# Performance work log

Hardware: AMD Instinct MI355X
Metric: run time of the kernel (lower is better)

The kernel has to match this reference:

```python
import jax, jax.numpy as jnp
import numpy as np

EMBED_DIM = 1024
NUM_HEADS = 16
HEAD_DIM = EMBED_DIM // NUM_HEADS  # 64
KERNEL_SIZE = 64


def apply_rotary_emb(x, freqs_cos, freqs_sin):
    # x: [B, L, H, D]; freqs: [L, D//2]
    x_r = x[..., 0::2]
    x_i = x[..., 1::2]
    cos = freqs_cos[None, :, None, :]
    sin = freqs_sin[None, :, None, :]
    out_r = x_r * cos - x_i * sin
    out_i = x_r * sin + x_i * cos
    return jnp.stack([out_r, out_i], axis=-1).reshape(x.shape)


def setup_inputs() -> dict:
    key = jax.random.key(0)
    ks = jax.random.split(key, 8)
    B, L = 4, 4096
    x = jax.random.normal(ks[0], (B, L, EMBED_DIM), dtype=jnp.float32)
    freqs_cos = jax.random.normal(ks[1], (L, HEAD_DIM // 2), dtype=jnp.float32)
    freqs_sin = jax.random.normal(ks[2], (L, HEAD_DIM // 2), dtype=jnp.float32)
    attention_mask = jnp.ones((B, L), dtype=jnp.float32)
    scale = 1.0 / np.sqrt(EMBED_DIM)
    Wqkv = jax.random.normal(ks[3], (EMBED_DIM, 3 * EMBED_DIM), dtype=jnp.float32) * scale
    bqkv = jnp.zeros((3 * EMBED_DIM,), dtype=jnp.float32)
    proj = jax.random.normal(ks[4], (NUM_HEADS, HEAD_DIM, KERNEL_SIZE), dtype=jnp.float32) / np.sqrt(HEAD_DIM)
    Wout = jax.random.normal(ks[5], (EMBED_DIM, EMBED_DIM), dtype=jnp.float32) * scale
    bout = jnp.zeros((EMBED_DIM,), dtype=jnp.float32)
    return {"x": x, "freqs_cos": freqs_cos, "freqs_sin": freqs_sin,
            "attention_mask": attention_mask, "Wqkv": Wqkv, "bqkv": bqkv,
            "proj": proj, "Wout": Wout, "bout": bout}


def reference(x, freqs_cos, freqs_sin, attention_mask, Wqkv, bqkv, proj, Wout, bout):
    B, L, E = x.shape
    H, D = NUM_HEADS, HEAD_DIM
    qkv = x @ Wqkv + bqkv  # [B, L, 3E]
    q, k, v = jnp.split(qkv, 3, axis=-1)
    q = q.reshape(B, L, H, D)
    k = k.reshape(B, L, H, D)
    v = v.reshape(B, L, H, D)
    q = apply_rotary_emb(q, freqs_cos, freqs_sin)
    k = apply_rotary_emb(k, freqs_cos, freqs_sin)
    q = q.transpose(0, 2, 1, 3)  # [B, H, L, D]
    k = k.transpose(0, 2, 1, 3)
    v = v.transpose(0, 2, 1, 3)
    q_prime = jax.nn.relu(jnp.einsum('bhld,hdm->bhlm', q, proj))
    k_prime = jax.nn.relu(jnp.einsum('bhld,hdm->bhlm', k, proj))
    mask = attention_mask[:, None, :, None]  # [B, 1, L, 1]
    k_prime = k_prime * mask
    v = v * mask
    kv = jnp.einsum('bhlm,bhld->bhmd', k_prime, v)      # [B, H, M, D]
    context = jnp.einsum('bhlm,bhmd->bhld', q_prime, kv)  # [B, H, L, D]
    k_sum = k_prime.sum(axis=2)  # [B, H, M]
    norm = jnp.einsum('bhlm,bhm->bhl', q_prime, k_sum)
    output = context / (norm[..., None] + 0.0001)
    output = output.transpose(0, 2, 1, 3).reshape(B, L, E)
    return output @ Wout + bout
```

## Files before the change

kernel.cpp:

```cpp
#include <hip/hip_runtime.h>

#define LSEQ   4096
#define ROWS   16384
#define EMBED  1024
#define NHEADS 16
#define HDIM   64
#define QKV_N  3072

typedef __attribute__((ext_vector_type(8))) short bf16x8;
typedef __attribute__((ext_vector_type(8))) unsigned short u16x8;
typedef __attribute__((ext_vector_type(4))) float f32x4;
typedef __attribute__((ext_vector_type(16))) float f32x16;

__device__ inline unsigned short bf16_rne(float x) {
    unsigned int u = __float_as_uint(x);
    unsigned int r = (u + 0x7fffu + ((u >> 16) & 1u)) >> 16;
    return (unsigned short)r;
}
__device__ inline float bf16_to_f32(unsigned short h) {
    return __uint_as_float(((unsigned int)h) << 16);
}

__device__ __forceinline__ int swz64(int row, int s) {
    return row * 64 + ((((s >> 3) ^ (row & 7))) << 3) + (s & 7);
}

__global__ __launch_bounds__(256)
void convert_hilo(const float* __restrict__ in, unsigned short* __restrict__ hi,
                  unsigned short* __restrict__ lo, int n)
{
    int i = (blockIdx.x * 256 + threadIdx.x) << 2;
    if (i >= n) return;
    float4 v = *reinterpret_cast<const float4*>(&in[i]);
    float a[4] = {v.x, v.y, v.z, v.w};
    unsigned short hh[4], ll[4];
    #pragma unroll
    for (int j = 0; j < 4; ++j) {
        hh[j] = bf16_rne(a[j]);
        ll[j] = bf16_rne(a[j] - bf16_to_f32(hh[j]));
    }
    *reinterpret_cast<ushort4*>(&hi[i]) = make_ushort4(hh[0], hh[1], hh[2], hh[3]);
    *reinterpret_cast<ushort4*>(&lo[i]) = make_ushort4(ll[0], ll[1], ll[2], ll[3]);
}

__global__ __launch_bounds__(256)
void convert_T_hilo(const float* __restrict__ in, unsigned short* __restrict__ hi,
                    unsigned short* __restrict__ lo, int K, int N)
{
    __shared__ float tile[64][65];
    const int n0 = blockIdx.x * 64, k0 = blockIdx.y * 64;
    const int t = threadIdx.x;
    #pragma unroll
    for (int i = 0; i < 16; ++i) {
        int idx = t + i * 256;
        int r = idx >> 6, c = idx & 63;
        tile[r][c] = in[(size_t)(k0 + r) * N + n0 + c];
    }
    __syncthreads();
    #pragma unroll
    for (int i = 0; i < 16; ++i) {
        int idx = t + i * 256;
        int r = idx >> 6, c = idx & 63;
        float v = tile[c][r];
        unsigned short h = bf16_rne(v);
        unsigned short l = bf16_rne(v - bf16_to_f32(h));
        size_t o = (size_t)(n0 + r) * K + k0 + c;
        hi[o] = h;
        lo[o] = l;
    }
}

__global__ __launch_bounds__(256)
void gemm3_kernel(const unsigned short* __restrict__ Ah, const unsigned short* __restrict__ Al,
                  const unsigned short* __restrict__ Bh, const unsigned short* __restrict__ Bl,
                  const float* __restrict__ bias, float* __restrict__ C,
                  int K, int ldc)
{
    __shared__ __align__(16) unsigned short lds[2][16384];

    const int t = threadIdx.x;
    const int wave = t >> 6, lane = t & 63;
    const int wr = wave >> 1, wc = wave & 1;
    const int rowBase = blockIdx.y * 128;
    const int colBase = blockIdx.x * 128;
    const int l31 = lane & 31, kg = lane >> 5;

    const unsigned short* src = (wave == 0) ? Ah : (wave == 1) ? Al : (wave == 2) ? Bh : Bl;
    const int tileRow0 = (wave < 2) ? rowBase : colBase;
    const int ldsOff = wave * 4096;
    const int sRow = lane >> 2;
    const int sChunk = (((lane & 3) ^ ((lane >> 3) & 3)) << 3);

    f32x16 acc[2][2] = {};
    const int NT = K >> 5;

    #pragma unroll
    for (int i = 0; i < 8; ++i) {
        const unsigned short* g = src + (size_t)(tileRow0 + i * 16 + sRow) * K + sChunk;
        __builtin_amdgcn_global_load_lds(
            (const __attribute__((address_space(1))) void*)g,
            (__attribute__((address_space(3))) void*)&lds[0][ldsOff + i * 512], 16, 0, 0);
    }
    __syncthreads();

    for (int tI = 0; tI < NT; ++tI) {
        const int cur = tI & 1;

        if (tI + 1 < NT) {
            const int k0 = (tI + 1) << 5;
            #pragma unroll
            for (int i = 0; i < 8; ++i) {
                const unsigned short* g =
                    src + (size_t)(tileRow0 + i * 16 + sRow) * K + k0 + sChunk;
                __builtin_amdgcn_global_load_lds(
                    (const __attribute__((address_space(1))) void*)g,
                    (__attribute__((address_space(3))) void*)&lds[cur ^ 1][ldsOff + i * 512], 16, 0, 0);
            }
        }

        bf16x8 ah[2][2], al[2][2], bh[2][2], bl[2][2];
        #pragma unroll
        for (int ks = 0; ks < 2; ++ks) {
            #pragma unroll
            for (int m = 0; m < 2; ++m) {
                int r = wr * 64 + m * 32 + l31;
                int off = r * 32 + ((((ks << 1) | kg) ^ ((r >> 1) & 3)) << 3);
                ah[ks][m] = *reinterpret_cast<const bf16x8*>(&lds[cur][off]);
                al[ks][m] = *reinterpret_cast<const bf16x8*>(&lds[cur][4096 + off]);
            }
            #pragma unroll
            for (int n = 0; n < 2; ++n) {
                int rb = wc * 64 + n * 32 + l31;
                int off = rb * 32 + ((((ks << 1) | kg) ^ ((rb >> 1) & 3)) << 3);
                bh[ks][n] = *reinterpret_cast<const bf16x8*>(&lds[cur][8192 + off]);
                bl[ks][n] = *reinterpret_cast<const bf16x8*>(&lds[cur][12288 + off]);
            }
        }
        #pragma unroll
        for (int ks = 0; ks < 2; ++ks)
            #pragma unroll
            for (int m = 0; m < 2; ++m)
                #pragma unroll
                for (int n = 0; n < 2; ++n) {
                    acc[m][n] = __builtin_amdgcn_mfma_f32_32x32x16_bf16(ah[ks][m], bh[ks][n], acc[m][n], 0, 0, 0);
                    acc[m][n] = __builtin_amdgcn_mfma_f32_32x32x16_bf16(ah[ks][m], bl[ks][n], acc[m][n], 0, 0, 0);
                    acc[m][n] = __builtin_amdgcn_mfma_f32_32x32x16_bf16(al[ks][m], bh[ks][n], acc[m][n], 0, 0, 0);
                }

        __syncthreads();
    }

    #pragma unroll
    for (int n = 0; n < 2; ++n) {
        const int col = colBase + wc * 64 + n * 32 + l31;
        const float bv = bias[col];
        #pragma unroll
        for (int m = 0; m < 2; ++m) {
            #pragma unroll
            for (int reg = 0; reg < 16; ++reg) {
                int row = rowBase + wr * 64 + m * 32 + (reg & 3) + 8 * (reg >> 2) + 4 * kg;
                C[(size_t)row * ldc + col] = acc[m][n][reg] + bv;
            }
        }
    }
}

__global__ __launch_bounds__(256)
void kv_mfma_kernel(const float* __restrict__ kvb, const float* __restrict__ cosb,
                    const float* __restrict__ sinb, const float* __restrict__ maskb,
                    const float* __restrict__ proj, float* __restrict__ partial)
{
    __shared__ __align__(16) char smem[66816];
    unsigned short* KR_h  = (unsigned short*)smem;
    unsigned short* KR_l  = (unsigned short*)(smem + 8192);
    float*          PS    = (float*)smem;
    unsigned short* PJT_h = (unsigned short*)(smem + 16384);
    unsigned short* PJT_l = (unsigned short*)(smem + 24576);
    unsigned short* KPT_h = (unsigned short*)(smem + 32768);
    unsigned short* KPT_l = (unsigned short*)(smem + 40960);
    unsigned short* VT_h  = (unsigned short*)(smem + 49152);
    unsigned short* VT_l  = (unsigned short*)(smem + 57344);
    float*          MS    = (float*)(smem + 65536);
    float*          KS    = (float*)(smem + 65792);

    const int chunk = blockIdx.x;
    const int hh    = blockIdx.y;
    const int t = threadIdx.x;
    const int w = t >> 6, lane = t & 63;
    const int fr = lane & 15, fq = lane >> 4;

    {
        int r = t >> 2, c0 = (t & 3) << 4;
        #pragma unroll
        for (int k = 0; k < 4; ++k)
            *reinterpret_cast<float4*>(&PS[r * 64 + c0 + k * 4]) =
                *reinterpret_cast<const float4*>(&proj[(size_t)hh * 4096 + r * 64 + c0 + k * 4]);
    }
    __syncthreads();
    {
        int m = t >> 2, d0 = (t & 3) << 4;
        unsigned short hb[16], lb[16];
        #pragma unroll
        for (int j = 0; j < 16; ++j) {
            float v = PS[(d0 + j) * 64 + m];
            hb[j] = bf16_rne(v);
            lb[j] = bf16_rne(v - bf16_to_f32(hb[j]));
        }
        #pragma unroll
        for (int cp = 0; cp < 2; ++cp) {
            u16x8 vh, vl;
            #pragma unroll
            for (int j = 0; j < 8; ++j) { vh[j] = hb[cp * 8 + j]; vl[j] = lb[cp * 8 + j]; }
            int sidx = swz64(m, d0 + cp * 8);
            *reinterpret_cast<u16x8*>(&PJT_h[sidx]) = vh;
            *reinterpret_cast<u16x8*>(&PJT_l[sidx]) = vl;
        }
    }
    __syncthreads();

    f32x4 acc2[4] = {};
    float ksacc[4] = {0.f, 0.f, 0.f, 0.f};

    for (int sub = 0; sub < 4; ++sub) {
        const int rowL = chunk * 256 + sub * 64;

        float4 vv[4];
        {
            int l = t >> 2, c0 = (t & 3) << 4;
            #pragma unroll
            for (int k2 = 0; k2 < 4; ++k2)
                vv[k2] = *reinterpret_cast<const float4*>(
                    &kvb[(size_t)(rowL + l) * 2048 + 1024 + hh * 64 + c0 + k2 * 4]);
        }
        #pragma unroll
        for (int i = 0; i < 8; ++i) {
            int p = t + (i << 8);
            int l = p >> 5, i2 = p & 31;
            size_t base = (size_t)(rowL + l) * 2048 + hh * 64 + 2 * i2;
            float kr = kvb[base], ki = kvb[base + 1];
            int crow = (rowL + l) & 4095;
            float c = cosb[(size_t)crow * 32 + i2];
            float s = sinb[(size_t)crow * 32 + i2];
            float xr = kr * c - ki * s;
            float xi = kr * s + ki * c;
            unsigned short h0 = bf16_rne(xr), h1 = bf16_rne(xi);
            unsigned short l0 = bf16_rne(xr - bf16_to_f32(h0));
            unsigned short l1 = bf16_rne(xi - bf16_to_f32(h1));
            int sidx = swz64(l, 2 * i2);
            *reinterpret_cast<unsigned int*>(&KR_h[sidx]) = (unsigned)h0 | ((unsigned)h1 << 16);
            *reinterpret_cast<unsigned int*>(&KR_l[sidx]) = (unsigned)l0 | ((unsigned)l1 << 16);
        }
        if (t < 64) MS[t] = maskb[rowL + t];
        __syncthreads();

        f32x4 acc1[4] = {};
        #pragma unroll
        for (int ks = 0; ks < 2; ++ks) {
            bf16x8 ah = *reinterpret_cast<const bf16x8*>(&KR_h[swz64(16 * w + fr, ks * 32 + fq * 8)]);
            bf16x8 al = *reinterpret_cast<const bf16x8*>(&KR_l[swz64(16 * w + fr, ks * 32 + fq * 8)]);
            #pragma unroll
            for (int n = 0; n < 4; ++n) {
                bf16x8 bh = *reinterpret_cast<const bf16x8*>(&PJT_h[swz64(16 * n + fr, ks * 32 + fq * 8)]);
                bf16x8 bl = *reinterpret_cast<const bf16x8*>(&PJT_l[swz64(16 * n + fr, ks * 32 + fq * 8)]);
                acc1[n] = __builtin_amdgcn_mfma_f32_16x16x32_bf16(ah, bh, acc1[n], 0, 0, 0);
                acc1[n] = __builtin_amdgcn_mfma_f32_16x16x32_bf16(ah, bl, acc1[n], 0, 0, 0);
                acc1[n] = __builtin_amdgcn_mfma_f32_16x16x32_bf16(al, bh, acc1[n], 0, 0, 0);
            }
        }
        #pragma unroll
        for (int n = 0; n < 4; ++n) {
            unsigned short hb[4], lb[4];
            float ssum = 0.f;
            #pragma unroll
            for (int r = 0; r < 4; ++r) {
                int l = 16 * w + fq * 4 + r;
                float kp = fmaxf(acc1[n][r], 0.f) * MS[l];
                ssum += kp;
                hb[r] = bf16_rne(kp);
                lb[r] = bf16_rne(kp - bf16_to_f32(hb[r]));
            }
            ksacc[n] += ssum;
            int sidx = swz64(16 * n + fr, 16 * w + fq * 4);
            *reinterpret_cast<ushort4*>(&KPT_h[sidx]) = make_ushort4(hb[0], hb[1], hb[2], hb[3]);
            *reinterpret_cast<ushort4*>(&KPT_l[sidx]) = make_ushort4(lb[0], lb[1], lb[2], lb[3]);
        }
        __syncthreads();

        {
            float* VS = PS;
            int l = t >> 2, c0 = (t & 3) << 4;
            float mv = MS[l];
            #pragma unroll
            for (int k2 = 0; k2 < 4; ++k2) {
                float4 q = vv[k2];
                q.x *= mv; q.y *= mv; q.z *= mv; q.w *= mv;
                *reinterpret_cast<float4*>(&VS[l * 64 + c0 + k2 * 4]) = q;
            }
        }
        __syncthreads();

        {
            float* VS = PS;
            int d = t >> 2, l0 = (t & 3) << 4;
            unsigned short hb[16], lb[16];
            #pragma unroll
            for (int j = 0; j < 16; ++j) {
                float v = VS[(l0 + j) * 64 + d];
                hb[j] = bf16_rne(v);
                lb[j] = bf16_rne(v - bf16_to_f32(hb[j]));
            }
            #pragma unroll
            for (int cp = 0; cp < 2; ++cp) {
                u16x8 vh, vl;
                #pragma unroll
                for (int j = 0; j < 8; ++j) { vh[j] = hb[cp * 8 + j]; vl[j] = lb[cp * 8 + j]; }
                int sidx = swz64(d, l0 + cp * 8);
                *reinterpret_cast<u16x8*>(&VT_h[sidx]) = vh;
                *reinterpret_cast<u16x8*>(&VT_l[sidx]) = vl;
            }
        }
        __syncthreads();

        #pragma unroll
        for (int ks = 0; ks < 2; ++ks) {
            bf16x8 ah = *reinterpret_cast<const bf16x8*>(&KPT_h[swz64(16 * w + fr, ks * 32 + fq * 8)]);
            bf16x8 al = *reinterpret_cast<const bf16x8*>(&KPT_l[swz64(16 * w + fr, ks * 32 + fq * 8)]);
            #pragma unroll
            for (int n = 0; n < 4; ++n) {
                bf16x8 bh = *reinterpret_cast<const bf16x8*>(&VT_h[swz64(16 * n + fr, ks * 32 + fq * 8)]);
                bf16x8 bl = *reinterpret_cast<const bf16x8*>(&VT_l[swz64(16 * n + fr, ks * 32 + fq * 8)]);
                acc2[n] = __builtin_amdgcn_mfma_f32_16x16x32_bf16(ah, bh, acc2[n], 0, 0, 0);
                acc2[n] = __builtin_amdgcn_mfma_f32_16x16x32_bf16(ah, bl, acc2[n], 0, 0, 0);
                acc2[n] = __builtin_amdgcn_mfma_f32_16x16x32_bf16(al, bh, acc2[n], 0, 0, 0);
            }
        }
    }

    #pragma unroll
    for (int n = 0; n < 4; ++n) {
        float v = ksacc[n];
        v += __shfl_xor(v, 16);
        v += __shfl_xor(v, 32);
        if (fq == 0) KS[w * 64 + 16 * n + fr] = v;
    }
    __syncthreads();

    float* dst = partial + ((size_t)hh * 64 + chunk) * 4160;
    #pragma unroll
    for (int n = 0; n < 4; ++n)
        #pragma unroll
        for (int r = 0; r < 4; ++r) {
            int m = 16 * w + fq * 4 + r;
            int d = 16 * n + fr;
            dst[m * 64 + d] = acc2[n][r];
        }
    if (t < 64)
        dst[4096 + t] = KS[t] + KS[64 + t] + KS[128 + t] + KS[192 + t];
}

__global__ __launch_bounds__(256)
void kv_reduce_kernel(const float* __restrict__ partial, float* __restrict__ kvout)
{
    const int bh = blockIdx.x;
    const int b = bh >> 4, h = bh & 15;
    const int seg = blockIdx.y;
    for (int idx = seg * 1040 + threadIdx.x; idx < (seg + 1) * 1040; idx += 256) {
        float s = 0.f;
        for (int c = 0; c < 16; ++c)
            s += partial[((size_t)h * 64 + b * 16 + c) * 4160 + idx];
        kvout[(size_t)bh * 4160 + idx] = s;
    }
}

__global__ __launch_bounds__(256)
void context_kernel(const float* __restrict__ qb, const float* __restrict__ cosb,
                    const float* __restrict__ sinb, const float* __restrict__ proj,
                    const float* __restrict__ kvsum, unsigned short* __restrict__ ch,
                    unsigned short* __restrict__ cl)
{
    const int lt = blockIdx.x;
    const int h  = blockIdx.y;
    const int t = threadIdx.x;
    const int bh = (lt >> 6) * 16 + h;

    __shared__ float bufA[64][68];
    __shared__ float qp[64][68];
    __shared__ float pj[64][64];
    __shared__ float ksum[64];

    for (int i = t; i < 1024; i += 256)
        *reinterpret_cast<float4*>(&pj[0][0] + (size_t)i * 4) =
            *reinterpret_cast<const float4*>(proj + (size_t)h * 4096 + (size_t)i * 4);
    if (t < 64) ksum[t] = kvsum[(size_t)bh * 4160 + 4096 + t];

    const int rowL = lt * 64;
    #pragma unroll
    for (int i = 0; i < 8; ++i) {
        int p = t + i * 256;
        int l = p >> 5, i2 = p & 31;
        size_t base = (size_t)(rowL + l) * 1024 + h * HDIM + 2 * i2;
        float qr = qb[base], qi = qb[base + 1];
        int crow = (rowL + l) & 4095;
        float c = cosb[(size_t)crow * 32 + i2];
        float s = sinb[(size_t)crow * 32 + i2];
        bufA[l][2 * i2]     = qr * c - qi * s;
        bufA[l][2 * i2 + 1] = qr * s + qi * c;
    }
    __syncthreads();

    {
        int l = t >> 2, m0 = (t & 3) << 4;
        float a[16] = {};
        for (int d = 0; d < 64; ++d) {
            float ql = bufA[l][d];
            const float* pr = &pj[d][m0];
            #pragma unroll
            for (int j = 0; j < 16; ++j) a[j] = fmaf(ql, pr[j], a[j]);
        }
        #pragma unroll
        for (int j = 0; j < 16; ++j) qp[l][m0 + j] = fmaxf(a[j], 0.f);
    }
    __syncthreads();

    #pragma unroll
    for (int i = 0; i < 4; ++i) {
        int idx = t + i * 256;
        int mm = idx >> 4, dd = (idx & 15) << 2;
        *reinterpret_cast<float4*>(&bufA[mm][dd]) =
            *reinterpret_cast<const float4*>(&kvsum[(size_t)bh * 4160 + mm * 64 + dd]);
    }
    __syncthreads();

    {
        int l = t >> 2, d0 = (t & 3) << 4;
        float a[16] = {};
        float nrm = 0.f;
        for (int mm = 0; mm < 64; ++mm) {
            float qv = qp[l][mm];
            nrm = fmaf(qv, ksum[mm], nrm);
            const float* kr = &bufA[mm][d0];
            #pragma unroll
            for (int j = 0; j < 16; ++j) a[j] = fmaf(qv, kr[j], a[j]);
        }
        float inv = 1.0f / (nrm + 1e-4f);
        size_t orow = (size_t)(rowL + l) * 1024 + h * HDIM + d0;
        #pragma unroll
        for (int j4 = 0; j4 < 4; ++j4) {
            unsigned short hh2[4], ll2[4];
            #pragma unroll
            for (int j = 0; j < 4; ++j) {
                float v = a[j4 * 4 + j] * inv;
                hh2[j] = bf16_rne(v);
                ll2[j] = bf16_rne(v - bf16_to_f32(hh2[j]));
            }
            *reinterpret_cast<ushort4*>(&ch[orow + j4 * 4]) = make_ushort4(hh2[0], hh2[1], hh2[2], hh2[3]);
            *reinterpret_cast<ushort4*>(&cl[orow + j4 * 4]) = make_ushort4(ll2[0], ll2[1], ll2[2], ll2[3]);
        }
    }
}

extern "C" void kernel_launch(void* const* d_in, const int* in_sizes, int n_in,
                              void* d_out, int out_size, void* d_ws, size_t ws_size,
                              hipStream_t stream)
{
    const float* x    = (const float*)d_in[0];
    const float* fcos = (const float*)d_in[1];
    const float* fsin = (const float*)d_in[2];
    const float* mask = (const float*)d_in[3];
    const float* Wqkv = (const float*)d_in[4];
    const float* bqkv = (const float*)d_in[5];
    const float* proj = (const float*)d_in[6];
    const float* Wout = (const float*)d_in[7];
    const float* bout = (const float*)d_in[8];
    float* out = (float*)d_out;

    float* W    = (float*)d_ws;
    float* XHL  = W + 4194304;
    float* KVQ  = XHL + 16777216;
    float* PART = KVQ + 33554432;
    float* KSUM = PART + 4259840;

    unsigned short* Wqh = (unsigned short*)W;
    unsigned short* Wql = Wqh + 3145728;
    unsigned short* Woh = Wql + 3145728;
    unsigned short* Wol = Woh + 1048576;
    unsigned short* xh  = (unsigned short*)XHL;
    unsigned short* xl  = xh + 16777216;

    convert_T_hilo<<<dim3(3072 / 64, 1024 / 64), 256, 0, stream>>>(Wqkv, Wqh, Wql, 1024, 3072);
    convert_T_hilo<<<dim3(1024 / 64, 1024 / 64), 256, 0, stream>>>(Wout, Woh, Wol, 1024, 1024);

    convert_hilo<<<16384, 256, 0, stream>>>(x, xh, xl, ROWS * EMBED);

    gemm3_kernel<<<dim3(2048 / 128, ROWS / 128), 256, 0, stream>>>(
        xh, xl, Wqh + (size_t)1024 * 1024, Wql + (size_t)1024 * 1024,
        bqkv + 1024, KVQ, 1024, 2048);

    kv_mfma_kernel<<<dim3(64, 16), 256, 0, stream>>>(KVQ, fcos, fsin, mask, proj, PART);

    kv_reduce_kernel<<<dim3(64, 4), 256, 0, stream>>>(PART, KSUM);

    gemm3_kernel<<<dim3(1024 / 128, ROWS / 128), 256, 0, stream>>>(
        xh, xl, Wqh, Wql, bqkv, KVQ, 1024, 1024);

    context_kernel<<<dim3(256, 16), 256, 0, stream>>>(
        KVQ, fcos, fsin, proj, KSUM, xh, xl);

    gemm3_kernel<<<dim3(1024 / 128, ROWS / 128), 256, 0, stream>>>(
        xh, xl, Woh, Wol, bout, out, 1024, 1024);
}
```

Measured before the change: 613.6 us.

## Enlarge split-bf16 GEMM tile to 256x256 with 8 waves and new LDS swizzle

The three-pass bf16 hi/lo GEMM now uses 256x256 output tiles with 512 threads, where each wave computes a 128x64 sub-tile (4x2 MFMA blocks) instead of 64x64. The LDS layout interleaves hi and lo halves per row (64 shorts per row, XOR swizzle on 8 groups), and all waves cooperatively load A and B. The goal is higher arithmetic intensity per global and LDS byte. The costs are doubled LDS (128 KB double-buffered), more accumulator registers, and fewer blocks, which could hurt occupancy and tail balance on smaller grids.

```diff
diff --git a/kernel.cpp b/kernel.cpp
--- a/kernel.cpp
+++ b/kernel.cpp
@@ -70,35 +70,39 @@
     }
 }
 
-__global__ __launch_bounds__(256)
+__global__ __launch_bounds__(512)
 void gemm3_kernel(const unsigned short* __restrict__ Ah, const unsigned short* __restrict__ Al,
                   const unsigned short* __restrict__ Bh, const unsigned short* __restrict__ Bl,
                   const float* __restrict__ bias, float* __restrict__ C,
                   int K, int ldc)
 {
-    __shared__ __align__(16) unsigned short lds[2][16384];
+    __shared__ __align__(16) unsigned short lds[2][32768];
 
     const int t = threadIdx.x;
     const int wave = t >> 6, lane = t & 63;
-    const int wr = wave >> 1, wc = wave & 1;
-    const int rowBase = blockIdx.y * 128;
-    const int colBase = blockIdx.x * 128;
+    const int wr = wave >> 2, wc = wave & 3;
+    const int rowBase = blockIdx.y * 256;
+    const int colBase = blockIdx.x * 256;
     const int l31 = lane & 31, kg = lane >> 5;
-
-    const unsigned short* src = (wave == 0) ? Ah : (wave == 1) ? Al : (wave == 2) ? Bh : Bl;
-    const int tileRow0 = (wave < 2) ? rowBase : colBase;
-    const int ldsOff = wave * 4096;
-    const int sRow = lane >> 2;
-    const int sChunk = (((lane & 3) ^ ((lane >> 3) & 3)) << 3);
-
-    f32x16 acc[2][2] = {};
+    const int r7 = l31 & 7;
+
+    const int sIsA = (wave < 4) ? 1 : 0;
+    const int lr = lane >> 3;
+    const int lc = lane & 7;
+    const int g  = lc ^ lr;
+    const unsigned short* sSrc = sIsA ? (g < 4 ? Ah : Al) : (g < 4 ? Bh : Bl);
+    const int gk = (g & 3) << 3;
+    const int tRow0 = (sIsA ? rowBase : colBase) + (wave & 3) * 64;
+    const int ldsOff = (sIsA ? 0 : 16384) + (wave & 3) * 4096;
+
+    f32x16 acc[4][2] = {};
     const int NT = K >> 5;
 
     #pragma unroll
     for (int i = 0; i < 8; ++i) {
-        const unsigned short* g = src + (size_t)(tileRow0 + i * 16 + sRow) * K + sChunk;
+        const unsigned short* gp = sSrc + (size_t)(tRow0 + i * 8 + lr) * K + gk;
         __builtin_amdgcn_global_load_lds(
-            (const __attribute__((address_space(1))) void*)g,
+            (const __attribute__((address_space(1))) void*)gp,
             (__attribute__((address_space(3))) void*)&lds[0][ldsOff + i * 512], 16, 0, 0);
     }
     __syncthreads();
@@ -110,42 +114,38 @@
             const int k0 = (tI + 1) << 5;
             #pragma unroll
             for (int i = 0; i < 8; ++i) {
-                const unsigned short* g =
-                    src + (size_t)(tileRow0 + i * 16 + sRow) * K + k0 + sChunk;
+                const unsigned short* gp = sSrc + (size_t)(tRow0 + i * 8 + lr) * K + k0 + gk;
                 __builtin_amdgcn_global_load_lds(
-                    (const __attribute__((address_space(1))) void*)g,
+                    (const __attribute__((address_space(1))) void*)gp,
                     (__attribute__((address_space(3))) void*)&lds[cur ^ 1][ldsOff + i * 512], 16, 0, 0);
             }
         }
 
-        bf16x8 ah[2][2], al[2][2], bh[2][2], bl[2][2];
         #pragma unroll
         for (int ks = 0; ks < 2; ++ks) {
-            #pragma unroll
-            for (int m = 0; m < 2; ++m) {
-                int r = wr * 64 + m * 32 + l31;
-                int off = r * 32 + ((((ks << 1) | kg) ^ ((r >> 1) & 3)) << 3);
-                ah[ks][m] = *reinterpret_cast<const bf16x8*>(&lds[cur][off]);
-                al[ks][m] = *reinterpret_cast<const bf16x8*>(&lds[cur][4096 + off]);
+            const int gh = ks * 2 + kg;
+            bf16x8 ah[4], al[4], bh[2], bl[2];
+            #pragma unroll
+            for (int m = 0; m < 4; ++m) {
+                int r = wr * 128 + m * 32 + l31;
+                ah[m] = *reinterpret_cast<const bf16x8*>(&lds[cur][r * 64 + ((gh ^ r7) << 3)]);
+                al[m] = *reinterpret_cast<const bf16x8*>(&lds[cur][r * 64 + (((gh + 4) ^ r7) << 3)]);
             }
             #pragma unroll
             for (int n = 0; n < 2; ++n) {
                 int rb = wc * 64 + n * 32 + l31;
-                int off = rb * 32 + ((((ks << 1) | kg) ^ ((rb >> 1) & 3)) << 3);
-                bh[ks][n] = *reinterpret_cast<const bf16x8*>(&lds[cur][8192 + off]);
-                bl[ks][n] = *reinterpret_cast<const bf16x8*>(&lds[cur][12288 + off]);
-            }
-        }
-        #pragma unroll
-        for (int ks = 0; ks < 2; ++ks)
-            #pragma unroll
-            for (int m = 0; m < 2; ++m)
+                bh[n] = *reinterpret_cast<const bf16x8*>(&lds[cur][16384 + rb * 64 + ((gh ^ r7) << 3)]);
+                bl[n] = *reinterpret_cast<const bf16x8*>(&lds[cur][16384 + rb * 64 + (((gh + 4) ^ r7) << 3)]);
+            }
+            #pragma unroll
+            for (int m = 0; m < 4; ++m)
                 #pragma unroll
                 for (int n = 0; n < 2; ++n) {
-                    acc[m][n] = __builtin_amdgcn_mfma_f32_32x32x16_bf16(ah[ks][m], bh[ks][n], acc[m][n], 0, 0, 0);
-                    acc[m][n] = __builtin_amdgcn_mfma_f32_32x32x16_bf16(ah[ks][m], bl[ks][n], acc[m][n], 0, 0, 0);
-                    acc[m][n] = __builtin_amdgcn_mfma_f32_32x32x16_bf16(al[ks][m], bh[ks][n], acc[m][n], 0, 0, 0);
+                    acc[m][n] = __builtin_amdgcn_mfma_f32_32x32x16_bf16(ah[m], bh[n], acc[m][n], 0, 0, 0);
+                    acc[m][n] = __builtin_amdgcn_mfma_f32_32x32x16_bf16(ah[m], bl[n], acc[m][n], 0, 0, 0);
+                    acc[m][n] = __builtin_amdgcn_mfma_f32_32x32x16_bf16(al[m], bh[n], acc[m][n], 0, 0, 0);
                 }
+        }
 
         __syncthreads();
     }
@@ -155,10 +155,10 @@
         const int col = colBase + wc * 64 + n * 32 + l31;
         const float bv = bias[col];
         #pragma unroll
-        for (int m = 0; m < 2; ++m) {
+        for (int m = 0; m < 4; ++m) {
             #pragma unroll
             for (int reg = 0; reg < 16; ++reg) {
-                int row = rowBase + wr * 64 + m * 32 + (reg & 3) + 8 * (reg >> 2) + 4 * kg;
+                int row = rowBase + wr * 128 + m * 32 + (reg & 3) + 8 * (reg >> 2) + 4 * kg;
                 C[(size_t)row * ldc + col] = acc[m][n][reg] + bv;
             }
         }
@@ -492,7 +492,7 @@
 
     convert_hilo<<<16384, 256, 0, stream>>>(x, xh, xl, ROWS * EMBED);
 
-    gemm3_kernel<<<dim3(2048 / 128, ROWS / 128), 256, 0, stream>>>(
+    gemm3_kernel<<<dim3(2048 / 256, ROWS / 256), 512, 0, stream>>>(
         xh, xl, Wqh + (size_t)1024 * 1024, Wql + (size_t)1024 * 1024,
         bqkv + 1024, KVQ, 1024, 2048);
 
@@ -500,12 +500,12 @@
 
     kv_reduce_kernel<<<dim3(64, 4), 256, 0, stream>>>(PART, KSUM);
 
-    gemm3_kernel<<<dim3(1024 / 128, ROWS / 128), 256, 0, stream>>>(
+    gemm3_kernel<<<dim3(1024 / 256, ROWS / 256), 512, 0, stream>>>(
         xh, xl, Wqh, Wql, bqkv, KVQ, 1024, 1024);
 
     context_kernel<<<dim3(256, 16), 256, 0, stream>>>(
         KVQ, fcos, fsin, proj, KSUM, xh, xl);
 
-    gemm3_kernel<<<dim3(1024 / 128, ROWS / 128), 256, 0, stream>>>(
+    gemm3_kernel<<<dim3(1024 / 256, ROWS / 256), 512, 0, stream>>>(
         xh, xl, Woh, Wol, bout, out, 1024, 1024);
 }
```

After: 550.7 us. 1.11x faster.
